# Performance work log

Measured on AMD Instinct MI355X. Metric: run time of the kernel, lower is better.

## Reference

```python
import math
import jax, jax.numpy as jnp
import numpy as np

B, T, C = 1, 4096, 1024
H, DH = 16, 64
BAND = 128

def setup_inputs() -> dict:
    key = jax.random.key(0)
    ks = jax.random.split(key, 5)
    scale = 0.02
    return {
        "x":  jax.random.normal(ks[0], (B, T, C), dtype=jnp.float32),
        "Wq": jax.random.normal(ks[1], (C, C), dtype=jnp.float32) * scale,
        "Wk": jax.random.normal(ks[2], (C, C), dtype=jnp.float32) * scale,
        "Wv": jax.random.normal(ks[3], (C, C), dtype=jnp.float32) * scale,
        "Wo": jax.random.normal(ks[4], (C, C), dtype=jnp.float32) * scale,
    }

def _band_causal_mask(T, band, dtype=jnp.bool_):
    # allowed iff j <= i and (i - j) < band
    i = jnp.arange(T)[:, None]
    j = jnp.arange(T)[None, :]
    return (j <= i) & ((i - j) < band)  # (T, T)

def reference(x, Wq, Wk, Wv, Wo):
    Bs, Ts, Cs = x.shape
    # nn.Linear: y = x @ W^T (bias=False)
    q = (x @ Wq.T).reshape(Bs, Ts, H, DH).transpose(0, 2, 1, 3)  # (B,H,T,Dh)
    k = (x @ Wk.T).reshape(Bs, Ts, H, DH).transpose(0, 2, 1, 3)
    v = (x @ Wv.T).reshape(Bs, Ts, H, DH).transpose(0, 2, 1, 3)
    att = jnp.einsum('bhid,bhjd->bhij', q, k) / math.sqrt(DH)      # (B,H,T,T)
    mask = _band_causal_mask(Ts, BAND)                              # (T,T)
    att = jnp.where(mask[None, None], att, jnp.finfo(att.dtype).min)
    P = jax.nn.softmax(att, axis=-1)
    y = jnp.einsum('bhij,bhjd->bhid', P, v)                         # (B,H,T,Dh)
    y = y.transpose(0, 2, 1, 3).reshape(Bs, Ts, Cs)                 # (B,T,C)
    return y @ Wo.T
```

## Files before the change

kernel.cpp:

```cpp
#include <hip/hip_runtime.h>
#include <hip/hip_bf16.h>
#include <stdint.h>

#define T_SEQ 4096
#define CDIM  1024
#define NH    16
#define DHEAD 64
#define BAND  128

typedef __bf16 bf16;
typedef __attribute__((ext_vector_type(8))) __bf16 bf16x8;
typedef __attribute__((ext_vector_type(4))) float  f32x4;

__device__ __forceinline__ void async_ld16(const bf16* g, bf16* l) {
    __builtin_amdgcn_global_load_lds(
        (__attribute__((address_space(1))) void*)g,
        (__attribute__((address_space(3))) void*)l, 16, 0, 0);
}

__global__ void cvt_all(const float* __restrict__ x,  const float* __restrict__ wq,
                        const float* __restrict__ wk, const float* __restrict__ wv,
                        const float* __restrict__ wo,
                        bf16* __restrict__ xb, bf16* __restrict__ wqkvb,
                        bf16* __restrict__ wob) {
    size_t i = (size_t)blockIdx.x * 256 + threadIdx.x;
    if (i < 4194304) { xb[i] = (bf16)x[i]; return; }
    size_t i2 = i - 4194304;
    if (i2 < 3145728) {
        int which = (int)(i2 >> 20);
        size_t off = i2 & 1048575;
        const float* src = (which == 0) ? wq : (which == 1 ? wk : wv);
        wqkvb[i2] = (bf16)src[off];
        return;
    }
    size_t i3 = i2 - 3145728;
    wob[i3] = (bf16)wo[i3];
}

__global__ __launch_bounds__(256) void gemm_qkv(
        const bf16* __restrict__ A, const bf16* __restrict__ B,
        bf16* __restrict__ qb, bf16* __restrict__ kb, bf16* __restrict__ vtb) {
    const int K = 1024;
    __shared__ __align__(16) bf16 lds_a[128 * 32];
    __shared__ __align__(16) bf16 lds_b[128 * 32];
    int t = threadIdx.x;
    int w = t >> 6, l = t & 63;
    int quad = l >> 4, col = l & 15;
    int bx = blockIdx.x;
    int bm = bx & 31, bn = bx >> 5;
    int m0 = bm * 128, n0 = bn * 128;
    int wm = (w >> 1) * 64, wn = (w & 1) * 64;

    f32x4 acc[4][4];
#pragma unroll
    for (int i = 0; i < 4; i++)
#pragma unroll
        for (int j = 0; j < 4; j++) acc[i][j] = (f32x4){0.f, 0.f, 0.f, 0.f};

    int c0 = t, c1 = 256 + t;
    int ra0 = c0 >> 2, ka0 = (c0 & 3) * 8;
    int ra1 = c1 >> 2, ka1 = (c1 & 3) * 8;
    bf16* la0 = lds_a + (size_t)(w * 64) * 8;
    bf16* la1 = lds_a + (size_t)(256 + w * 64) * 8;
    bf16* lb0 = lds_b + (size_t)(w * 64) * 8;
    bf16* lb1 = lds_b + (size_t)(256 + w * 64) * 8;

    for (int k0 = 0; k0 < K; k0 += 32) {
        async_ld16(A + (size_t)(m0 + ra0) * K + k0 + ka0, la0);
        async_ld16(A + (size_t)(m0 + ra1) * K + k0 + ka1, la1);
        async_ld16(B + (size_t)(n0 + ra0) * K + k0 + ka0, lb0);
        async_ld16(B + (size_t)(n0 + ra1) * K + k0 + ka1, lb1);
        __syncthreads();
        const bf16x8* pa = (const bf16x8*)lds_a;
        const bf16x8* pb = (const bf16x8*)lds_b;
        bf16x8 af[4], bfr[4];
#pragma unroll
        for (int i = 0; i < 4; i++) af[i]  = pa[(wm + i * 16 + col) * 4 + quad];
#pragma unroll
        for (int j = 0; j < 4; j++) bfr[j] = pb[(wn + j * 16 + col) * 4 + quad];
#pragma unroll
        for (int i = 0; i < 4; i++)
#pragma unroll
            for (int j = 0; j < 4; j++)
                acc[i][j] = __builtin_amdgcn_mfma_f32_16x16x32_bf16(af[i], bfr[j], acc[i][j], 0, 0, 0);
        __syncthreads();
    }
#pragma unroll
    for (int i = 0; i < 4; i++)
#pragma unroll
        for (int j = 0; j < 4; j++) {
            int mbase = m0 + wm + i * 16 + quad * 4;
            int ncol = n0 + wn + j * 16 + col;
            int which = ncol >> 10;
            int o = ncol & 1023;
            int h = o >> 6, d = o & 63;
#pragma unroll
            for (int r = 0; r < 4; r++) {
                int tt = mbase + r;
                bf16 v = (bf16)acc[i][j][r];
                if (which == 0)       qb[((size_t)(h * T_SEQ + tt)) * 64 + d] = v;
                else if (which == 1)  kb[((size_t)(h * T_SEQ + tt)) * 64 + d] = v;
                else                  vtb[((size_t)(h * 64 + d)) * T_SEQ + tt] = v;
            }
        }
}

__global__ __launch_bounds__(256) void attn(
        const bf16* __restrict__ qbuf, const bf16* __restrict__ kbuf,
        const bf16* __restrict__ vtbuf, bf16* __restrict__ yb) {
    __shared__ __align__(16) bf16 p_lds[4 * 32 * 128];
    int t = threadIdx.x;
    int w = t >> 6, l = t & 63;
    int quad = l >> 4, col = l & 15;
    int bx = blockIdx.x;
    int h = bx >> 5;
    int qt = bx & 31;
    int i0 = qt * 128;
    int rowbase = i0 + w * 32;

    const bf16* Q  = qbuf  + (size_t)h * T_SEQ * 64;
    const bf16* Kp = kbuf  + (size_t)h * T_SEQ * 64;
    const bf16* Vt = vtbuf + (size_t)h * 64 * T_SEQ;

    f32x4 o_acc[2][4];
#pragma unroll
    for (int mi = 0; mi < 2; mi++)
#pragma unroll
        for (int di = 0; di < 4; di++) o_acc[mi][di] = (f32x4){0.f, 0.f, 0.f, 0.f};
    float m_run[2][4], l_run[2][4];
#pragma unroll
    for (int mi = 0; mi < 2; mi++)
#pragma unroll
        for (int r = 0; r < 4; r++) { m_run[mi][r] = -3.0e38f; l_run[mi][r] = 0.f; }

    bf16x8 qf[2][2];
#pragma unroll
    for (int mi = 0; mi < 2; mi++)
#pragma unroll
        for (int kk = 0; kk < 2; kk++)
            qf[mi][kk] = *(const bf16x8*)(Q + (size_t)(rowbase + mi * 16 + col) * 64 + kk * 32 + quad * 8);

    bf16* myp = p_lds + (size_t)w * (32 * 128);

    int ktstart = (qt == 0) ? 1 : 0;
    for (int kt = ktstart; kt < 2; kt++) {
        int j0 = i0 + (kt - 1) * 128;
        f32x4 s[2][8];
#pragma unroll
        for (int mi = 0; mi < 2; mi++)
#pragma unroll
            for (int nj = 0; nj < 8; nj++) s[mi][nj] = (f32x4){0.f, 0.f, 0.f, 0.f};
#pragma unroll
        for (int nj = 0; nj < 8; nj++)
#pragma unroll
            for (int kk = 0; kk < 2; kk++) {
                bf16x8 kf = *(const bf16x8*)(Kp + (size_t)(j0 + nj * 16 + col) * 64 + kk * 32 + quad * 8);
#pragma unroll
                for (int mi = 0; mi < 2; mi++)
                    s[mi][nj] = __builtin_amdgcn_mfma_f32_16x16x32_bf16(qf[mi][kk], kf, s[mi][nj], 0, 0, 0);
            }
#pragma unroll
        for (int mi = 0; mi < 2; mi++)
#pragma unroll
            for (int nj = 0; nj < 8; nj++)
#pragma unroll
                for (int r = 0; r < 4; r++) {
                    int ii = rowbase + mi * 16 + quad * 4 + r;
                    int jj = j0 + nj * 16 + col;
                    bool ok = (kt == 1) ? (jj <= ii) : (ii - jj < BAND);
                    s[mi][nj][r] = ok ? s[mi][nj][r] * 0.125f : -3.0e38f;
                }
#pragma unroll
        for (int mi = 0; mi < 2; mi++)
#pragma unroll
            for (int r = 0; r < 4; r++) {
                float mx = -3.0e38f;
#pragma unroll
                for (int nj = 0; nj < 8; nj++) mx = fmaxf(mx, s[mi][nj][r]);
                mx = fmaxf(mx, __shfl_xor(mx, 1));
                mx = fmaxf(mx, __shfl_xor(mx, 2));
                mx = fmaxf(mx, __shfl_xor(mx, 4));
                mx = fmaxf(mx, __shfl_xor(mx, 8));
                float mnew = fmaxf(m_run[mi][r], mx);
                float alpha = __expf(m_run[mi][r] - mnew);
                m_run[mi][r] = mnew;
                float rs = 0.f;
#pragma unroll
                for (int nj = 0; nj < 8; nj++) {
                    float p = __expf(s[mi][nj][r] - mnew);
                    s[mi][nj][r] = p;
                    rs += p;
                }
                rs += __shfl_xor(rs, 1);
                rs += __shfl_xor(rs, 2);
                rs += __shfl_xor(rs, 4);
                rs += __shfl_xor(rs, 8);
                l_run[mi][r] = l_run[mi][r] * alpha + rs;
#pragma unroll
                for (int di = 0; di < 4; di++) o_acc[mi][di][r] *= alpha;
            }
#pragma unroll
        for (int mi = 0; mi < 2; mi++)
#pragma unroll
            for (int nj = 0; nj < 8; nj++)
#pragma unroll
                for (int r = 0; r < 4; r++) {
                    int row = mi * 16 + quad * 4 + r;
                    int c = nj * 16 + col;
                    myp[row * 128 + c] = (bf16)s[mi][nj][r];
                }
#pragma unroll
        for (int kj = 0; kj < 4; kj++) {
            bf16x8 pf[2];
#pragma unroll
            for (int mi = 0; mi < 2; mi++)
                pf[mi] = *(const bf16x8*)(myp + (mi * 16 + col) * 128 + kj * 32 + quad * 8);
#pragma unroll
            for (int di = 0; di < 4; di++) {
                bf16x8 vf = *(const bf16x8*)(Vt + (size_t)(di * 16 + col) * T_SEQ + j0 + kj * 32 + quad * 8);
#pragma unroll
                for (int mi = 0; mi < 2; mi++)
                    o_acc[mi][di] = __builtin_amdgcn_mfma_f32_16x16x32_bf16(pf[mi], vf, o_acc[mi][di], 0, 0, 0);
            }
        }
    }
#pragma unroll
    for (int mi = 0; mi < 2; mi++)
#pragma unroll
        for (int di = 0; di < 4; di++)
#pragma unroll
            for (int r = 0; r < 4; r++) {
                int tt = rowbase + mi * 16 + quad * 4 + r;
                int c = h * 64 + di * 16 + col;
                yb[(size_t)tt * CDIM + c] = (bf16)(o_acc[mi][di][r] / l_run[mi][r]);
            }
}

__global__ __launch_bounds__(256) void gemm_proj(
        const bf16* __restrict__ A, const bf16* __restrict__ B,
        float* __restrict__ Cout) {
    const int K = 1024;
    __shared__ __align__(16) bf16 lds_a[128 * 32];
    __shared__ __align__(16) bf16 lds_b[128 * 32];
    int t = threadIdx.x;
    int w = t >> 6, l = t & 63;
    int quad = l >> 4, col = l & 15;
    int bx = blockIdx.x;
    int bm = bx & 31, bn = bx >> 5;
    int m0 = bm * 128, n0 = bn * 128;
    int wm = (w >> 1) * 64, wn = (w & 1) * 64;

    f32x4 acc[4][4];
#pragma unroll
    for (int i = 0; i < 4; i++)
#pragma unroll
        for (int j = 0; j < 4; j++) acc[i][j] = (f32x4){0.f, 0.f, 0.f, 0.f};

    int c0 = t, c1 = 256 + t;
    int ra0 = c0 >> 2, ka0 = (c0 & 3) * 8;
    int ra1 = c1 >> 2, ka1 = (c1 & 3) * 8;
    bf16* la0 = lds_a + (size_t)(w * 64) * 8;
    bf16* la1 = lds_a + (size_t)(256 + w * 64) * 8;
    bf16* lb0 = lds_b + (size_t)(w * 64) * 8;
    bf16* lb1 = lds_b + (size_t)(256 + w * 64) * 8;

    for (int k0 = 0; k0 < K; k0 += 32) {
        async_ld16(A + (size_t)(m0 + ra0) * K + k0 + ka0, la0);
        async_ld16(A + (size_t)(m0 + ra1) * K + k0 + ka1, la1);
        async_ld16(B + (size_t)(n0 + ra0) * K + k0 + ka0, lb0);
        async_ld16(B + (size_t)(n0 + ra1) * K + k0 + ka1, lb1);
        __syncthreads();
        const bf16x8* pa = (const bf16x8*)lds_a;
        const bf16x8* pb = (const bf16x8*)lds_b;
        bf16x8 af[4], bfr[4];
#pragma unroll
        for (int i = 0; i < 4; i++) af[i]  = pa[(wm + i * 16 + col) * 4 + quad];
#pragma unroll
        for (int j = 0; j < 4; j++) bfr[j] = pb[(wn + j * 16 + col) * 4 + quad];
#pragma unroll
        for (int i = 0; i < 4; i++)
#pragma unroll
            for (int j = 0; j < 4; j++)
                acc[i][j] = __builtin_amdgcn_mfma_f32_16x16x32_bf16(af[i], bfr[j], acc[i][j], 0, 0, 0);
        __syncthreads();
    }
#pragma unroll
    for (int i = 0; i < 4; i++)
#pragma unroll
        for (int j = 0; j < 4; j++) {
            int mbase = m0 + wm + i * 16 + quad * 4;
            int ncol = n0 + wn + j * 16 + col;
#pragma unroll
            for (int r = 0; r < 4; r++)
                Cout[(size_t)(mbase + r) * CDIM + ncol] = acc[i][j][r];
        }
}

extern "C" void kernel_launch(void* const* d_in, const int* in_sizes, int n_in,
                              void* d_out, int out_size, void* d_ws, size_t ws_size,
                              hipStream_t stream) {
    const float* x  = (const float*)d_in[0];
    const float* Wq = (const float*)d_in[1];
    const float* Wk = (const float*)d_in[2];
    const float* Wv = (const float*)d_in[3];
    const float* Wo = (const float*)d_in[4];
    float* out = (float*)d_out;

    char* ws = (char*)d_ws;
    bf16* xb    = (bf16*)(ws);
    bf16* wqkvb = (bf16*)(ws + ((size_t)8  << 20));
    bf16* wob   = (bf16*)(ws + ((size_t)14 << 20));
    bf16* qb    = (bf16*)(ws + ((size_t)16 << 20));
    bf16* kb    = (bf16*)(ws + ((size_t)24 << 20));
    bf16* vtb   = (bf16*)(ws + ((size_t)32 << 20));
    bf16* yb    = (bf16*)(ws + ((size_t)40 << 20));

    cvt_all<<<32768, 256, 0, stream>>>(x, Wq, Wk, Wv, Wo, xb, wqkvb, wob);
    gemm_qkv<<<768, 256, 0, stream>>>(xb, wqkvb, qb, kb, vtb);
    attn<<<512, 256, 0, stream>>>(qb, kb, vtb, yb);
    gemm_proj<<<256, 256, 0, stream>>>(yb, wob, out);
}
```

Measured before the change: 173.1 us.

## Vectorize conversion, narrow attention to per-warp band window, halve proj GEMM tile

The fp32-to-bf16 conversion kernel now handles 8 elements per thread with float4 loads and a 16-byte store, so it launches 8x fewer blocks. Attention drops the two-tile online softmax and has each warp compute a 160-key window aligned to its own 32 rows. This skips fully masked key columns and removes the rescaling, and the P buffer in LDS gets a padded stride. The output-projection GEMM uses 64x128 tiles, doubling the block count to 512 for better CU occupancy, at the cost of less data reuse per block.

```diff
diff --git a/kernel.cpp b/kernel.cpp
--- a/kernel.cpp
+++ b/kernel.cpp
@@ -23,18 +23,25 @@
                         const float* __restrict__ wo,
                         bf16* __restrict__ xb, bf16* __restrict__ wqkvb,
                         bf16* __restrict__ wob) {
-    size_t i = (size_t)blockIdx.x * 256 + threadIdx.x;
-    if (i < 4194304) { xb[i] = (bf16)x[i]; return; }
-    size_t i2 = i - 4194304;
-    if (i2 < 3145728) {
+    size_t g = (size_t)blockIdx.x * 256 + threadIdx.x;
+    const float* s; bf16* d;
+    if (g < 524288) {
+        s = x + g * 8; d = xb + g * 8;
+    } else if (g < 917504) {
+        size_t i2 = (g - 524288) * 8;
         int which = (int)(i2 >> 20);
-        size_t off = i2 & 1048575;
-        const float* src = (which == 0) ? wq : (which == 1 ? wk : wv);
-        wqkvb[i2] = (bf16)src[off];
-        return;
-    }
-    size_t i3 = i2 - 3145728;
-    wob[i3] = (bf16)wo[i3];
+        s = ((which == 0) ? wq : (which == 1) ? wk : wv) + (i2 & 1048575);
+        d = wqkvb + i2;
+    } else {
+        size_t i3 = (g - 917504) * 8;
+        s = wo + i3; d = wob + i3;
+    }
+    const float4* sv = (const float4*)s;
+    float4 a = sv[0], b = sv[1];
+    bf16x8 o;
+    o[0] = (bf16)a.x; o[1] = (bf16)a.y; o[2] = (bf16)a.z; o[3] = (bf16)a.w;
+    o[4] = (bf16)b.x; o[5] = (bf16)b.y; o[6] = (bf16)b.z; o[7] = (bf16)b.w;
+    *(bf16x8*)d = o;
 }
 
 __global__ __launch_bounds__(256) void gemm_qkv(
@@ -105,34 +112,25 @@
         }
 }
 
+#define PSTR 168
+
 __global__ __launch_bounds__(256) void attn(
         const bf16* __restrict__ qbuf, const bf16* __restrict__ kbuf,
         const bf16* __restrict__ vtbuf, bf16* __restrict__ yb) {
-    __shared__ __align__(16) bf16 p_lds[4 * 32 * 128];
+    __shared__ __align__(16) bf16 p_lds[4 * 32 * PSTR];
     int t = threadIdx.x;
     int w = t >> 6, l = t & 63;
     int quad = l >> 4, col = l & 15;
-    int bx = blockIdx.x;
-    int h = bx >> 5;
-    int qt = bx & 31;
+    int h = blockIdx.x >> 5;
+    int qt = blockIdx.x & 31;
     int i0 = qt * 128;
     int rowbase = i0 + w * 32;
+    int jbase = rowbase - 128;
 
     const bf16* Q  = qbuf  + (size_t)h * T_SEQ * 64;
     const bf16* Kp = kbuf  + (size_t)h * T_SEQ * 64;
     const bf16* Vt = vtbuf + (size_t)h * 64 * T_SEQ;
 
-    f32x4 o_acc[2][4];
-#pragma unroll
-    for (int mi = 0; mi < 2; mi++)
-#pragma unroll
-        for (int di = 0; di < 4; di++) o_acc[mi][di] = (f32x4){0.f, 0.f, 0.f, 0.f};
-    float m_run[2][4], l_run[2][4];
-#pragma unroll
-    for (int mi = 0; mi < 2; mi++)
-#pragma unroll
-        for (int r = 0; r < 4; r++) { m_run[mi][r] = -3.0e38f; l_run[mi][r] = 0.f; }
-
     bf16x8 qf[2][2];
 #pragma unroll
     for (int mi = 0; mi < 2; mi++)
@@ -140,90 +138,88 @@
         for (int kk = 0; kk < 2; kk++)
             qf[mi][kk] = *(const bf16x8*)(Q + (size_t)(rowbase + mi * 16 + col) * 64 + kk * 32 + quad * 8);
 
-    bf16* myp = p_lds + (size_t)w * (32 * 128);
-
-    int ktstart = (qt == 0) ? 1 : 0;
-    for (int kt = ktstart; kt < 2; kt++) {
-        int j0 = i0 + (kt - 1) * 128;
-        f32x4 s[2][8];
+    f32x4 s[2][10];
+#pragma unroll
+    for (int mi = 0; mi < 2; mi++)
+#pragma unroll
+        for (int nj = 0; nj < 10; nj++) s[mi][nj] = (f32x4){0.f, 0.f, 0.f, 0.f};
+#pragma unroll
+    for (int nj = 0; nj < 10; nj++) {
+        int jr = jbase + nj * 16 + col;
+        int jl = jr < 0 ? 0 : jr;
+#pragma unroll
+        for (int kk = 0; kk < 2; kk++) {
+            bf16x8 kf = *(const bf16x8*)(Kp + (size_t)jl * 64 + kk * 32 + quad * 8);
+#pragma unroll
+            for (int mi = 0; mi < 2; mi++)
+                s[mi][nj] = __builtin_amdgcn_mfma_f32_16x16x32_bf16(qf[mi][kk], kf, s[mi][nj], 0, 0, 0);
+        }
+    }
+
+    float l_run[2][4];
+#pragma unroll
+    for (int mi = 0; mi < 2; mi++)
+#pragma unroll
+        for (int r = 0; r < 4; r++) {
+            int ii = rowbase + mi * 16 + quad * 4 + r;
+            float mx = -3.0e38f;
+#pragma unroll
+            for (int nj = 0; nj < 10; nj++) {
+                int jj = jbase + nj * 16 + col;
+                bool ok = (jj >= 0) && ((unsigned)(ii - jj) < (unsigned)BAND);
+                float v = ok ? s[mi][nj][r] * 0.125f : -3.0e38f;
+                s[mi][nj][r] = v;
+                mx = fmaxf(mx, v);
+            }
+            mx = fmaxf(mx, __shfl_xor(mx, 1));
+            mx = fmaxf(mx, __shfl_xor(mx, 2));
+            mx = fmaxf(mx, __shfl_xor(mx, 4));
+            mx = fmaxf(mx, __shfl_xor(mx, 8));
+            float rs = 0.f;
+#pragma unroll
+            for (int nj = 0; nj < 10; nj++) {
+                float p = __expf(s[mi][nj][r] - mx);
+                s[mi][nj][r] = p;
+                rs += p;
+            }
+            rs += __shfl_xor(rs, 1);
+            rs += __shfl_xor(rs, 2);
+            rs += __shfl_xor(rs, 4);
+            rs += __shfl_xor(rs, 8);
+            l_run[mi][r] = rs;
+        }
+
+    bf16* myp = p_lds + (size_t)w * (32 * PSTR);
+#pragma unroll
+    for (int mi = 0; mi < 2; mi++)
+#pragma unroll
+        for (int nj = 0; nj < 10; nj++)
+#pragma unroll
+            for (int r = 0; r < 4; r++)
+                myp[(mi * 16 + quad * 4 + r) * PSTR + nj * 16 + col] = (bf16)s[mi][nj][r];
+
+    f32x4 o_acc[2][4];
+#pragma unroll
+    for (int mi = 0; mi < 2; mi++)
+#pragma unroll
+        for (int di = 0; di < 4; di++) o_acc[mi][di] = (f32x4){0.f, 0.f, 0.f, 0.f};
+#pragma unroll
+    for (int kj = 0; kj < 5; kj++) {
+        int jv = jbase + kj * 32 + quad * 8;
+        int jvc = jv < 0 ? 0 : jv;
+        bf16x8 pf[2];
 #pragma unroll
         for (int mi = 0; mi < 2; mi++)
-#pragma unroll
-            for (int nj = 0; nj < 8; nj++) s[mi][nj] = (f32x4){0.f, 0.f, 0.f, 0.f};
-#pragma unroll
-        for (int nj = 0; nj < 8; nj++)
-#pragma unroll
-            for (int kk = 0; kk < 2; kk++) {
-                bf16x8 kf = *(const bf16x8*)(Kp + (size_t)(j0 + nj * 16 + col) * 64 + kk * 32 + quad * 8);
-#pragma unroll
-                for (int mi = 0; mi < 2; mi++)
-                    s[mi][nj] = __builtin_amdgcn_mfma_f32_16x16x32_bf16(qf[mi][kk], kf, s[mi][nj], 0, 0, 0);
-            }
-#pragma unroll
-        for (int mi = 0; mi < 2; mi++)
-#pragma unroll
-            for (int nj = 0; nj < 8; nj++)
-#pragma unroll
-                for (int r = 0; r < 4; r++) {
-                    int ii = rowbase + mi * 16 + quad * 4 + r;
-                    int jj = j0 + nj * 16 + col;
-                    bool ok = (kt == 1) ? (jj <= ii) : (ii - jj < BAND);
-                    s[mi][nj][r] = ok ? s[mi][nj][r] * 0.125f : -3.0e38f;
-                }
-#pragma unroll
-        for (int mi = 0; mi < 2; mi++)
-#pragma unroll
-            for (int r = 0; r < 4; r++) {
-                float mx = -3.0e38f;
-#pragma unroll
-                for (int nj = 0; nj < 8; nj++) mx = fmaxf(mx, s[mi][nj][r]);
-                mx = fmaxf(mx, __shfl_xor(mx, 1));
-                mx = fmaxf(mx, __shfl_xor(mx, 2));
-                mx = fmaxf(mx, __shfl_xor(mx, 4));
-                mx = fmaxf(mx, __shfl_xor(mx, 8));
-                float mnew = fmaxf(m_run[mi][r], mx);
-                float alpha = __expf(m_run[mi][r] - mnew);
-                m_run[mi][r] = mnew;
-                float rs = 0.f;
-#pragma unroll
-                for (int nj = 0; nj < 8; nj++) {
-                    float p = __expf(s[mi][nj][r] - mnew);
-                    s[mi][nj][r] = p;
-                    rs += p;
-                }
-                rs += __shfl_xor(rs, 1);
-                rs += __shfl_xor(rs, 2);
-                rs += __shfl_xor(rs, 4);
-                rs += __shfl_xor(rs, 8);
-                l_run[mi][r] = l_run[mi][r] * alpha + rs;
-#pragma unroll
-                for (int di = 0; di < 4; di++) o_acc[mi][di][r] *= alpha;
-            }
-#pragma unroll
-        for (int mi = 0; mi < 2; mi++)
-#pragma unroll
-            for (int nj = 0; nj < 8; nj++)
-#pragma unroll
-                for (int r = 0; r < 4; r++) {
-                    int row = mi * 16 + quad * 4 + r;
-                    int c = nj * 16 + col;
-                    myp[row * 128 + c] = (bf16)s[mi][nj][r];
-                }
-#pragma unroll
-        for (int kj = 0; kj < 4; kj++) {
-            bf16x8 pf[2];
+            pf[mi] = *(const bf16x8*)(myp + (mi * 16 + col) * PSTR + kj * 32 + quad * 8);
+#pragma unroll
+        for (int di = 0; di < 4; di++) {
+            bf16x8 vf = *(const bf16x8*)(Vt + (size_t)(di * 16 + col) * T_SEQ + jvc);
 #pragma unroll
             for (int mi = 0; mi < 2; mi++)
-                pf[mi] = *(const bf16x8*)(myp + (mi * 16 + col) * 128 + kj * 32 + quad * 8);
-#pragma unroll
-            for (int di = 0; di < 4; di++) {
-                bf16x8 vf = *(const bf16x8*)(Vt + (size_t)(di * 16 + col) * T_SEQ + j0 + kj * 32 + quad * 8);
-#pragma unroll
-                for (int mi = 0; mi < 2; mi++)
-                    o_acc[mi][di] = __builtin_amdgcn_mfma_f32_16x16x32_bf16(pf[mi], vf, o_acc[mi][di], 0, 0, 0);
-            }
-        }
-    }
+                o_acc[mi][di] = __builtin_amdgcn_mfma_f32_16x16x32_bf16(pf[mi], vf, o_acc[mi][di], 0, 0, 0);
+        }
+    }
+
 #pragma unroll
     for (int mi = 0; mi < 2; mi++)
 #pragma unroll
@@ -240,52 +236,51 @@
         const bf16* __restrict__ A, const bf16* __restrict__ B,
         float* __restrict__ Cout) {
     const int K = 1024;
-    __shared__ __align__(16) bf16 lds_a[128 * 32];
+    __shared__ __align__(16) bf16 lds_a[64 * 32];
     __shared__ __align__(16) bf16 lds_b[128 * 32];
     int t = threadIdx.x;
     int w = t >> 6, l = t & 63;
     int quad = l >> 4, col = l & 15;
     int bx = blockIdx.x;
-    int bm = bx & 31, bn = bx >> 5;
-    int m0 = bm * 128, n0 = bn * 128;
-    int wm = (w >> 1) * 64, wn = (w & 1) * 64;
-
-    f32x4 acc[4][4];
-#pragma unroll
-    for (int i = 0; i < 4; i++)
+    int bm = bx & 63, bn = bx >> 6;
+    int m0 = bm * 64, n0 = bn * 128;
+    int wm = (w >> 1) * 32, wn = (w & 1) * 64;
+
+    f32x4 acc[2][4];
+#pragma unroll
+    for (int i = 0; i < 2; i++)
 #pragma unroll
         for (int j = 0; j < 4; j++) acc[i][j] = (f32x4){0.f, 0.f, 0.f, 0.f};
 
-    int c0 = t, c1 = 256 + t;
-    int ra0 = c0 >> 2, ka0 = (c0 & 3) * 8;
-    int ra1 = c1 >> 2, ka1 = (c1 & 3) * 8;
+    int ra0 = t >> 2, ka0 = (t & 3) * 8;
+    int c1 = t, c2 = 256 + t;
+    int rb1 = c1 >> 2, kb1 = (c1 & 3) * 8;
+    int rb2 = c2 >> 2, kb2 = (c2 & 3) * 8;
     bf16* la0 = lds_a + (size_t)(w * 64) * 8;
-    bf16* la1 = lds_a + (size_t)(256 + w * 64) * 8;
-    bf16* lb0 = lds_b + (size_t)(w * 64) * 8;
-    bf16* lb1 = lds_b + (size_t)(256 + w * 64) * 8;
+    bf16* lb1 = lds_b + (size_t)(w * 64) * 8;
+    bf16* lb2 = lds_b + (size_t)(256 + w * 64) * 8;
 
     for (int k0 = 0; k0 < K; k0 += 32) {
         async_ld16(A + (size_t)(m0 + ra0) * K + k0 + ka0, la0);
-        async_ld16(A + (size_t)(m0 + ra1) * K + k0 + ka1, la1);
-        async_ld16(B + (size_t)(n0 + ra0) * K + k0 + ka0, lb0);
-        async_ld16(B + (size_t)(n0 + ra1) * K + k0 + ka1, lb1);
+        async_ld16(B + (size_t)(n0 + rb1) * K + k0 + kb1, lb1);
+        async_ld16(B + (size_t)(n0 + rb2) * K + k0 + kb2, lb2);
         __syncthreads();
         const bf16x8* pa = (const bf16x8*)lds_a;
         const bf16x8* pb = (const bf16x8*)lds_b;
-        bf16x8 af[4], bfr[4];
-#pragma unroll
-        for (int i = 0; i < 4; i++) af[i]  = pa[(wm + i * 16 + col) * 4 + quad];
+        bf16x8 af[2], bfr[4];
+#pragma unroll
+        for (int i = 0; i < 2; i++) af[i]  = pa[(wm + i * 16 + col) * 4 + quad];
 #pragma unroll
         for (int j = 0; j < 4; j++) bfr[j] = pb[(wn + j * 16 + col) * 4 + quad];
 #pragma unroll
-        for (int i = 0; i < 4; i++)
+        for (int i = 0; i < 2; i++)
 #pragma unroll
             for (int j = 0; j < 4; j++)
                 acc[i][j] = __builtin_amdgcn_mfma_f32_16x16x32_bf16(af[i], bfr[j], acc[i][j], 0, 0, 0);
         __syncthreads();
     }
 #pragma unroll
-    for (int i = 0; i < 4; i++)
+    for (int i = 0; i < 2; i++)
 #pragma unroll
         for (int j = 0; j < 4; j++) {
             int mbase = m0 + wm + i * 16 + quad * 4;
@@ -315,8 +310,8 @@
     bf16* vtb   = (bf16*)(ws + ((size_t)32 << 20));
     bf16* yb    = (bf16*)(ws + ((size_t)40 << 20));
 
-    cvt_all<<<32768, 256, 0, stream>>>(x, Wq, Wk, Wv, Wo, xb, wqkvb, wob);
+    cvt_all<<<4096, 256, 0, stream>>>(x, Wq, Wk, Wv, Wo, xb, wqkvb, wob);
     gemm_qkv<<<768, 256, 0, stream>>>(xb, wqkvb, qb, kb, vtb);
     attn<<<512, 256, 0, stream>>>(qb, kb, vtb, yb);
-    gemm_proj<<<256, 256, 0, stream>>>(yb, wob, out);
-}
+    gemm_proj<<<512, 256, 0, stream>>>(yb, wob, out);
+}
```

New measurement: 155.9 us. 1.11x faster.
